# Optimization experiments

Measured on AMD Instinct MI355X. Metric: run time of the kernel, lower is better.

The kernel has to match this reference:

```python
import jax, jax.numpy as jnp
import numpy as np

N_NODES = 50000
N_EDGES = 1600000
DIM = 512


def setup_inputs() -> dict:
    key = jax.random.key(0)
    k1, k2, k3, k4, k5 = jax.random.split(key, 5)
    x = jax.random.normal(k1, (N_NODES, DIM), dtype=jnp.float32)
    adj_rows = jax.random.randint(k2, (N_EDGES,), 0, N_NODES, dtype=jnp.int32)
    adj_cols = jax.random.randint(k3, (N_EDGES,), 0, N_NODES, dtype=jnp.int32)
    adj_vals = jax.random.uniform(k4, (N_EDGES,), dtype=jnp.float32)
    # fc1 weight [out_dim, in_dim], kaiming-normal-ish init
    weight = jax.random.normal(k5, (DIM, DIM), dtype=jnp.float32) * np.float32(np.sqrt(2.0 / DIM))
    scale = jnp.full((1,), 1.5, dtype=jnp.float32)
    return {"x": x, "adj_rows": adj_rows, "adj_cols": adj_cols,
            "adj_vals": adj_vals, "weight": weight, "scale": scale}


def reference(x, adj_rows, adj_cols, adj_vals, weight, scale):
    # dropout in eval mode -> identity
    N, D = x.shape
    # dense linear: y = x @ W^T
    y = jnp.einsum('nd,od->no', x, weight)
    # sparse adj @ y  (COO SpMM via gather + segment_sum)
    y = jax.ops.segment_sum(adj_vals[:, None] * y[adj_cols], adj_rows,
                            num_segments=N)
    # sp_norm: mean-center over nodes, scale by global RMS^{-1} * (1+scale) * sqrt(D)
    y_t = y - jnp.mean(y, axis=0, keepdims=True)
    y_norm = jnp.mean(jnp.sum(y_t * y_t, axis=1)) ** -0.5
    y = y_t * y_norm * (1.0 + scale) * jnp.float32(np.sqrt(D))
    # activation (relu), then residual (input_dim == output_dim)
    y = jax.nn.relu(y)
    return y + x
```

## Files before the change

### kernel.cpp

```cpp
#include <hip/hip_runtime.h>
#include <hip/hip_bf16.h>
#include <cstdint>
#include <cstddef>

#define N_NODES 50000
#define DIM 512
#define N_EDGES 1600000
#define NT 25
#define NB (N_NODES * NT)
#define GPANELS 391
#define NSHAD 8

typedef __bf16 bf16;
typedef __bf16 bf16x8 __attribute__((ext_vector_type(8)));
typedef __bf16 bf16x4 __attribute__((ext_vector_type(4)));
typedef float floatx4 __attribute__((ext_vector_type(4)));

__global__ void cast_kernel(const float* __restrict__ in, bf16* __restrict__ out, int n4) {
    int i = blockIdx.x * blockDim.x + threadIdx.x;
    if (i >= n4) return;
    float4 v = reinterpret_cast<const float4*>(in)[i];
    bf16x4 o;
    o[0] = (bf16)v.x; o[1] = (bf16)v.y; o[2] = (bf16)v.z; o[3] = (bf16)v.w;
    reinterpret_cast<bf16x4*>(out)[i] = o;
}

__global__ void hist_kernel(const int* __restrict__ rows, const int* __restrict__ cols,
                            int* __restrict__ cnt, int E) {
    int i = blockIdx.x * blockDim.x + threadIdx.x;
    if (i < E) {
        int key = rows[i] * NT + (cols[i] >> 11);
        atomicAdd(&cnt[key], 1);
    }
}

__global__ __launch_bounds__(1024) void scanA_kernel(const int* __restrict__ cnt,
                                                     int* __restrict__ row_start,
                                                     int* __restrict__ blksum, int n) {
    const int t = threadIdx.x;
    int i = blockIdx.x * 1024 + t;
    int v = (i < n) ? cnt[i] : 0;
    int s = v;
#pragma unroll
    for (int off = 1; off < 64; off <<= 1) {
        int u = __shfl_up(s, off, 64);
        if ((t & 63) >= off) s += u;
    }
    __shared__ int wsum[16];
    if ((t & 63) == 63) wsum[t >> 6] = s;
    __syncthreads();
    if (t < 16) {
        int w = wsum[t];
#pragma unroll
        for (int off = 1; off < 16; off <<= 1) {
            int u = __shfl_up(w, off, 16);
            if (t >= off) w += u;
        }
        wsum[t] = w;
    }
    __syncthreads();
    int base = (t >= 64) ? wsum[(t >> 6) - 1] : 0;
    int incl = s + base;
    if (i < n) row_start[i] = incl - v;
    if (t == 1023) blksum[blockIdx.x] = incl;
}

__global__ __launch_bounds__(1024) void scanB_kernel(const int* __restrict__ blksum,
                                                     int* __restrict__ blkoff, int nb) {
    __shared__ int s[1024];
    const int t = threadIdx.x;
    const int base = t * 2;
    int a = (base < nb) ? blksum[base] : 0;
    int b = (base + 1 < nb) ? blksum[base + 1] : 0;
    s[t] = a + b;
    __syncthreads();
    for (int off = 1; off < 1024; off <<= 1) {
        int u = (t >= off) ? s[t - off] : 0;
        __syncthreads();
        s[t] += u;
        __syncthreads();
    }
    int excl = (t == 0) ? 0 : s[t - 1];
    if (base < nb) blkoff[base] = excl;
    if (base + 1 < nb) blkoff[base + 1] = excl + a;
}

__global__ __launch_bounds__(1024) void scanC_kernel(int* __restrict__ row_start,
                                                     const int* __restrict__ blkoff,
                                                     int* __restrict__ cursor, int n) {
    int i = blockIdx.x * 1024 + threadIdx.x;
    if (i >= n) return;
    int v = row_start[i] + blkoff[i >> 10];
    row_start[i] = v;
    cursor[i] = v;
    if (i == n - 1) row_start[n] = N_EDGES;
}

__global__ void scatter_kernel(const int* __restrict__ rows, const int* __restrict__ cols,
                               const float* __restrict__ vals, int* __restrict__ cursor,
                               int2* __restrict__ ecv, int E) {
    int i = blockIdx.x * blockDim.x + threadIdx.x;
    if (i >= E) return;
    int c = cols[i];
    int key = rows[i] * NT + (c >> 11);
    int p = atomicAdd(&cursor[key], 1);
    ecv[p] = make_int2(c, __float_as_int(vals[i]));
}

__global__ __launch_bounds__(256) void gemm_kernel(const bf16* __restrict__ A,
                                                   const bf16* __restrict__ B,
                                                   bf16* __restrict__ C) {
    __shared__ bf16 lA[128 * 32];
    __shared__ bf16 lB[128 * 32];
    const int d = blockIdx.x;
    const int p = (d & 7) + ((d >> 5) << 3);
    const int c = (d >> 3) & 3;
    if (p >= GPANELS) return;
    const int t = threadIdx.x;
    const int wave = t >> 6;
    const int lane = t & 63;
    const int rowBase = p * 128;
    const int colBase = c * 128;
    const int wm = (wave >> 1) * 64;
    const int wn = (wave & 1) * 64;
    floatx4 acc[4][4] = {};

    const int r_a = t >> 2;
    const int kk = (t & 3) * 8;

    const int l15 = lane & 15;
    const int koff = (lane >> 4) * 8;

    for (int k0 = 0; k0 < DIM; k0 += 32) {
#pragma unroll
        for (int j = 0; j < 2; j++) {
            int row = rowBase + r_a + j * 64;
            if (row > N_NODES - 1) row = N_NODES - 1;
            const bf16* g = A + (size_t)row * DIM + k0 + kk;
            bf16* l = lA + wave * 512 + j * 2048;
            __builtin_amdgcn_global_load_lds(
                (const __attribute__((address_space(1))) void*)g,
                (__attribute__((address_space(3))) void*)l, 16, 0, 0);
        }
#pragma unroll
        for (int j = 0; j < 2; j++) {
            int row = colBase + r_a + j * 64;
            const bf16* g = B + (size_t)row * DIM + k0 + kk;
            bf16* l = lB + wave * 512 + j * 2048;
            __builtin_amdgcn_global_load_lds(
                (const __attribute__((address_space(1))) void*)g,
                (__attribute__((address_space(3))) void*)l, 16, 0, 0);
        }
        __syncthreads();
        bf16x8 af[4], bfr[4];
#pragma unroll
        for (int i = 0; i < 4; i++)
            af[i] = *reinterpret_cast<const bf16x8*>(lA + (wm + i * 16 + l15) * 32 + koff);
#pragma unroll
        for (int j = 0; j < 4; j++)
            bfr[j] = *reinterpret_cast<const bf16x8*>(lB + (wn + j * 16 + l15) * 32 + koff);
#pragma unroll
        for (int i = 0; i < 4; i++)
#pragma unroll
            for (int j = 0; j < 4; j++)
                acc[i][j] = __builtin_amdgcn_mfma_f32_16x16x32_bf16(af[i], bfr[j], acc[i][j], 0, 0, 0);
        __syncthreads();
    }
    const int rquad = (lane >> 4) * 4;
#pragma unroll
    for (int i = 0; i < 4; i++) {
#pragma unroll
        for (int reg = 0; reg < 4; reg++) {
            int gr = rowBase + wm + i * 16 + rquad + reg;
            if (gr >= N_NODES) continue;
#pragma unroll
            for (int j = 0; j < 4; j++) {
                int gc = colBase + wn + j * 16 + l15;
                C[(size_t)gr * DIM + gc] = (bf16)acc[i][j][reg];
            }
        }
    }
}

__device__ __forceinline__ float blo(uint32_t w) { return __uint_as_float(w << 16); }
__device__ __forceinline__ float bhi(uint32_t w) { return __uint_as_float(w & 0xffff0000u); }

__device__ __forceinline__ void fmac8(float* acc, float v, const uint4& w) {
    acc[0] += v * blo(w.x); acc[1] += v * bhi(w.x);
    acc[2] += v * blo(w.y); acc[3] += v * bhi(w.y);
    acc[4] += v * blo(w.z); acc[5] += v * bhi(w.z);
    acc[6] += v * blo(w.w); acc[7] += v * bhi(w.w);
}

__global__ __launch_bounds__(256) void spmm_kernel(const int* __restrict__ row_start,
                                                   const int2* __restrict__ ecv,
                                                   const bf16* __restrict__ y,
                                                   float* __restrict__ y2) {
    const int wave = threadIdx.x >> 6;
    const int lane = threadIdx.x & 63;
    const int r = blockIdx.x * 4 + wave;
    const int s = row_start[r * NT];
    const int e = row_start[(r + 1) * NT];
    float acc[8] = {0.f, 0.f, 0.f, 0.f, 0.f, 0.f, 0.f, 0.f};
    const uint32_t* yb = reinterpret_cast<const uint32_t*>(y);

    int i = s;
    for (; i + 3 < e; i += 4) {
        int2 e0 = ecv[i], e1 = ecv[i + 1], e2 = ecv[i + 2], e3 = ecv[i + 3];
        uint4 w0 = *reinterpret_cast<const uint4*>(yb + (size_t)e0.x * 256 + lane * 4);
        uint4 w1 = *reinterpret_cast<const uint4*>(yb + (size_t)e1.x * 256 + lane * 4);
        uint4 w2 = *reinterpret_cast<const uint4*>(yb + (size_t)e2.x * 256 + lane * 4);
        uint4 w3 = *reinterpret_cast<const uint4*>(yb + (size_t)e3.x * 256 + lane * 4);
        fmac8(acc, __int_as_float(e0.y), w0);
        fmac8(acc, __int_as_float(e1.y), w1);
        fmac8(acc, __int_as_float(e2.y), w2);
        fmac8(acc, __int_as_float(e3.y), w3);
    }
    for (; i < e; i++) {
        int2 e0 = ecv[i];
        uint4 w0 = *reinterpret_cast<const uint4*>(yb + (size_t)e0.x * 256 + lane * 4);
        fmac8(acc, __int_as_float(e0.y), w0);
    }
    float4* out = reinterpret_cast<float4*>(y2 + (size_t)r * DIM + lane * 8);
    out[0] = make_float4(acc[0], acc[1], acc[2], acc[3]);
    out[1] = make_float4(acc[4], acc[5], acc[6], acc[7]);
}

#define RED_GRID 512
#define RED_CHUNK 16
__global__ __launch_bounds__(256) void reduce_kernel(const float* __restrict__ y2,
                                                     float* __restrict__ colsumS,
                                                     float* __restrict__ totsqS) {
    const int t = threadIdx.x;
    const int d2 = t * 2;
    float c0 = 0.f, c1 = 0.f, sq = 0.f;
    for (int r0 = blockIdx.x * RED_CHUNK; r0 < N_NODES; r0 += RED_GRID * RED_CHUNK) {
        float2 v[RED_CHUNK];
#pragma unroll
        for (int j = 0; j < RED_CHUNK; j++) {
            int r = r0 + j;
            v[j] = (r < N_NODES)
                       ? *reinterpret_cast<const float2*>(y2 + (size_t)r * DIM + d2)
                       : make_float2(0.f, 0.f);
        }
#pragma unroll
        for (int j = 0; j < RED_CHUNK; j++) {
            c0 += v[j].x;
            c1 += v[j].y;
            sq += v[j].x * v[j].x + v[j].y * v[j].y;
        }
    }
    const int sh = blockIdx.x & (NSHAD - 1);
    atomicAdd(&colsumS[sh * DIM + d2], c0);
    atomicAdd(&colsumS[sh * DIM + d2 + 1], c1);
    __shared__ float ssq[256];
    ssq[t] = sq;
    __syncthreads();
    for (int off = 128; off > 0; off >>= 1) {
        if (t < off) ssq[t] += ssq[t + off];
        __syncthreads();
    }
    if (t == 0) atomicAdd(&totsqS[sh], ssq[0]);
}

__global__ void scalar_kernel(const float* __restrict__ colsumS, const float* __restrict__ totsqS,
                              const float* __restrict__ scale, float* __restrict__ sfac,
                              float* __restrict__ colsum) {
    __shared__ float sm[512];
    const int t = threadIdx.x;
    float s = 0.f;
#pragma unroll
    for (int c = 0; c < NSHAD; c++) s += colsumS[c * DIM + t];
    colsum[t] = s;
    float mu = s * (1.0f / N_NODES);
    sm[t] = mu * mu;
    __syncthreads();
    for (int off = 256; off > 0; off >>= 1) {
        if (t < off) sm[t] += sm[t + off];
        __syncthreads();
    }
    if (t == 0) {
        float tq = 0.f;
#pragma unroll
        for (int c = 0; c < NSHAD; c++) tq += totsqS[c];
        float var = tq * (1.0f / N_NODES) - sm[0];
        sfac[0] = rsqrtf(var) * (1.0f + scale[0]) * sqrtf((float)DIM);
    }
}

__global__ void final_kernel(float* __restrict__ y2, const float* __restrict__ x,
                             const float* __restrict__ colsum, const float* __restrict__ sfac,
                             int n4) {
    int i = blockIdx.x * blockDim.x + threadIdx.x;
    if (i >= n4) return;
    const float invN = 1.0f / N_NODES;
    float4 v = reinterpret_cast<float4*>(y2)[i];
    float4 xv = reinterpret_cast<const float4*>(x)[i];
    float4 mu = reinterpret_cast<const float4*>(colsum)[i & 127];
    float s = sfac[0];
    v.x = fmaxf((v.x - mu.x * invN) * s, 0.0f) + xv.x;
    v.y = fmaxf((v.y - mu.y * invN) * s, 0.0f) + xv.y;
    v.z = fmaxf((v.z - mu.z * invN) * s, 0.0f) + xv.z;
    v.w = fmaxf((v.w - mu.w * invN) * s, 0.0f) + xv.w;
    reinterpret_cast<float4*>(y2)[i] = v;
}

extern "C" void kernel_launch(void* const* d_in, const int* in_sizes, int n_in,
                              void* d_out, int out_size, void* d_ws, size_t ws_size,
                              hipStream_t stream) {
    const float* x        = (const float*)d_in[0];
    const int*   adj_rows = (const int*)d_in[1];
    const int*   adj_cols = (const int*)d_in[2];
    const float* adj_vals = (const float*)d_in[3];
    const float* weight   = (const float*)d_in[4];
    const float* scale    = (const float*)d_in[5];
    float* out = (float*)d_out;

    char* ws = (char*)d_ws;
    size_t off = 0;
    auto alloc = [&](size_t b) {
        char* p = ws + off;
        off += (b + 255) & ~(size_t)255;
        return p;
    };
    const int nblk = (NB + 1023) / 1024;
    bf16*  xb        = (bf16*)alloc((size_t)N_NODES * DIM * 2);
    int2*  ecv       = (int2*)xb;
    bf16*  Wb        = (bf16*)alloc((size_t)DIM * DIM * 2);
    bf16*  y         = (bf16*)alloc((size_t)N_NODES * DIM * 2);
    int*   cnt       = (int*)alloc((size_t)NB * 4);
    int*   cursor    = cnt;
    int*   row_start = (int*)alloc((size_t)(NB + 1) * 4);
    int*   blksum    = (int*)alloc((size_t)nblk * 4);
    int*   blkoff    = (int*)alloc((size_t)nblk * 4);
    float* colsumS   = (float*)alloc((size_t)NSHAD * DIM * 4);
    float* totsqS    = (float*)alloc((size_t)NSHAD * 4);
    float* colsum    = (float*)alloc(512 * 4);
    float* sfac      = (float*)alloc(4);
    (void)ws_size; (void)in_sizes; (void)n_in; (void)out_size;

    hipMemsetAsync(cnt, 0, (size_t)NB * 4, stream);
    hipMemsetAsync(colsumS, 0, (size_t)NSHAD * DIM * 4 + 256, stream);

    const int n4x = N_NODES * DIM / 4;
    const int n4w = DIM * DIM / 4;
    cast_kernel<<<(n4x + 255) / 256, 256, 0, stream>>>(x, xb, n4x);
    cast_kernel<<<(n4w + 255) / 256, 256, 0, stream>>>(weight, Wb, n4w);

    gemm_kernel<<<1568, 256, 0, stream>>>(xb, Wb, y);

    hist_kernel<<<(N_EDGES + 255) / 256, 256, 0, stream>>>(adj_rows, adj_cols, cnt, N_EDGES);
    scanA_kernel<<<nblk, 1024, 0, stream>>>(cnt, row_start, blksum, NB);
    scanB_kernel<<<1, 1024, 0, stream>>>(blksum, blkoff, nblk);
    scanC_kernel<<<nblk, 1024, 0, stream>>>(row_start, blkoff, cursor, NB);
    scatter_kernel<<<(N_EDGES + 255) / 256, 256, 0, stream>>>(adj_rows, adj_cols, adj_vals,
                                                              cursor, ecv, N_EDGES);

    spmm_kernel<<<N_NODES / 4, 256, 0, stream>>>(row_start, ecv, y, out);

    reduce_kernel<<<RED_GRID, 256, 0, stream>>>(out, colsumS, totsqS);
    scalar_kernel<<<1, 512, 0, stream>>>(colsumS, totsqS, scale, sfac, colsum);
    final_kernel<<<(n4x + 255) / 256, 256, 0, stream>>>(out, x, colsum, sfac, n4x);
}
```

Baseline: 684.9 us.

## Double-buffer GEMM LDS tiles and fuse casts and memsets into one prep kernel

The bf16 GEMM now keeps two LDS buffers. It issues the global-to-LDS loads for the next K slice before computing MFMAs on the current one, and the K loop is fully unrolled. The goal is to hide global load latency behind the matrix math, at the cost of doubling LDS use per block, which may lower occupancy. Separately, the two cast launches and the two hipMemsetAsync calls are merged into a single prep kernel that casts x and W and zeroes the histogram and statistics buffers, removing launch and memset overhead.

```diff
diff --git a/kernel.cpp b/kernel.cpp
--- a/kernel.cpp
+++ b/kernel.cpp
@@ -16,13 +16,25 @@
 typedef __bf16 bf16x4 __attribute__((ext_vector_type(4)));
 typedef float floatx4 __attribute__((ext_vector_type(4)));
 
-__global__ void cast_kernel(const float* __restrict__ in, bf16* __restrict__ out, int n4) {
+__global__ void prep_kernel(const float* __restrict__ x, bf16* __restrict__ xb,
+                            const float* __restrict__ w, bf16* __restrict__ wb,
+                            int4* __restrict__ cnt4, float4* __restrict__ stats4,
+                            int n4x, int n4w) {
     int i = blockIdx.x * blockDim.x + threadIdx.x;
-    if (i >= n4) return;
-    float4 v = reinterpret_cast<const float4*>(in)[i];
-    bf16x4 o;
-    o[0] = (bf16)v.x; o[1] = (bf16)v.y; o[2] = (bf16)v.z; o[3] = (bf16)v.w;
-    reinterpret_cast<bf16x4*>(out)[i] = o;
+    if (i < n4x) {
+        float4 v = reinterpret_cast<const float4*>(x)[i];
+        bf16x4 o;
+        o[0] = (bf16)v.x; o[1] = (bf16)v.y; o[2] = (bf16)v.z; o[3] = (bf16)v.w;
+        reinterpret_cast<bf16x4*>(xb)[i] = o;
+    }
+    if (i < n4w) {
+        float4 v = reinterpret_cast<const float4*>(w)[i];
+        bf16x4 o;
+        o[0] = (bf16)v.x; o[1] = (bf16)v.y; o[2] = (bf16)v.z; o[3] = (bf16)v.w;
+        reinterpret_cast<bf16x4*>(wb)[i] = o;
+    }
+    if (i < NB / 4) cnt4[i] = make_int4(0, 0, 0, 0);
+    if (i < 1026) stats4[i] = make_float4(0.f, 0.f, 0.f, 0.f);
 }
 
 __global__ void hist_kernel(const int* __restrict__ rows, const int* __restrict__ cols,
@@ -110,8 +122,8 @@
 __global__ __launch_bounds__(256) void gemm_kernel(const bf16* __restrict__ A,
                                                    const bf16* __restrict__ B,
                                                    bf16* __restrict__ C) {
-    __shared__ bf16 lA[128 * 32];
-    __shared__ bf16 lB[128 * 32];
+    __shared__ bf16 lA[2][128 * 32];
+    __shared__ bf16 lB[2][128 * 32];
     const int d = blockIdx.x;
     const int p = (d & 7) + ((d >> 5) << 3);
     const int c = (d >> 3) & 3;
@@ -127,38 +139,47 @@
 
     const int r_a = t >> 2;
     const int kk = (t & 3) * 8;
-
     const int l15 = lane & 15;
     const int koff = (lane >> 4) * 8;
 
-    for (int k0 = 0; k0 < DIM; k0 += 32) {
-#pragma unroll
-        for (int j = 0; j < 2; j++) {
-            int row = rowBase + r_a + j * 64;
-            if (row > N_NODES - 1) row = N_NODES - 1;
-            const bf16* g = A + (size_t)row * DIM + k0 + kk;
-            bf16* l = lA + wave * 512 + j * 2048;
-            __builtin_amdgcn_global_load_lds(
-                (const __attribute__((address_space(1))) void*)g,
-                (__attribute__((address_space(3))) void*)l, 16, 0, 0);
-        }
-#pragma unroll
-        for (int j = 0; j < 2; j++) {
-            int row = colBase + r_a + j * 64;
-            const bf16* g = B + (size_t)row * DIM + k0 + kk;
-            bf16* l = lB + wave * 512 + j * 2048;
-            __builtin_amdgcn_global_load_lds(
-                (const __attribute__((address_space(1))) void*)g,
-                (__attribute__((address_space(3))) void*)l, 16, 0, 0);
-        }
-        __syncthreads();
+    int arow0 = rowBase + r_a;
+    if (arow0 > N_NODES - 1) arow0 = N_NODES - 1;
+    int arow1 = rowBase + r_a + 64;
+    if (arow1 > N_NODES - 1) arow1 = N_NODES - 1;
+    const bf16* gA0 = A + (size_t)arow0 * DIM + kk;
+    const bf16* gA1 = A + (size_t)arow1 * DIM + kk;
+    const bf16* gB0 = B + (size_t)(colBase + r_a) * DIM + kk;
+    const bf16* gB1 = B + (size_t)(colBase + r_a + 64) * DIM + kk;
+
+    auto STAGE = [&](int b, int kc) {
+        const int ko = kc * 32;
+        __builtin_amdgcn_global_load_lds(
+            (const __attribute__((address_space(1))) void*)(gA0 + ko),
+            (__attribute__((address_space(3))) void*)(&lA[b][wave * 512]), 16, 0, 0);
+        __builtin_amdgcn_global_load_lds(
+            (const __attribute__((address_space(1))) void*)(gA1 + ko),
+            (__attribute__((address_space(3))) void*)(&lA[b][wave * 512 + 2048]), 16, 0, 0);
+        __builtin_amdgcn_global_load_lds(
+            (const __attribute__((address_space(1))) void*)(gB0 + ko),
+            (__attribute__((address_space(3))) void*)(&lB[b][wave * 512]), 16, 0, 0);
+        __builtin_amdgcn_global_load_lds(
+            (const __attribute__((address_space(1))) void*)(gB1 + ko),
+            (__attribute__((address_space(3))) void*)(&lB[b][wave * 512 + 2048]), 16, 0, 0);
+    };
+
+    STAGE(0, 0);
+    __syncthreads();
+#pragma unroll
+    for (int s = 0; s < 16; s++) {
+        if (s + 1 < 16) STAGE((s + 1) & 1, s + 1);
+        const int b = s & 1;
         bf16x8 af[4], bfr[4];
 #pragma unroll
         for (int i = 0; i < 4; i++)
-            af[i] = *reinterpret_cast<const bf16x8*>(lA + (wm + i * 16 + l15) * 32 + koff);
+            af[i] = *reinterpret_cast<const bf16x8*>(&lA[b][(wm + i * 16 + l15) * 32 + koff]);
 #pragma unroll
         for (int j = 0; j < 4; j++)
-            bfr[j] = *reinterpret_cast<const bf16x8*>(lB + (wn + j * 16 + l15) * 32 + koff);
+            bfr[j] = *reinterpret_cast<const bf16x8*>(&lB[b][(wn + j * 16 + l15) * 32 + koff]);
 #pragma unroll
         for (int i = 0; i < 4; i++)
 #pragma unroll
@@ -339,13 +360,12 @@
     float* sfac      = (float*)alloc(4);
     (void)ws_size; (void)in_sizes; (void)n_in; (void)out_size;
 
-    hipMemsetAsync(cnt, 0, (size_t)NB * 4, stream);
-    hipMemsetAsync(colsumS, 0, (size_t)NSHAD * DIM * 4 + 256, stream);
-
     const int n4x = N_NODES * DIM / 4;
     const int n4w = DIM * DIM / 4;
-    cast_kernel<<<(n4x + 255) / 256, 256, 0, stream>>>(x, xb, n4x);
-    cast_kernel<<<(n4w + 255) / 256, 256, 0, stream>>>(weight, Wb, n4w);
+
+    prep_kernel<<<(n4x + 255) / 256, 256, 0, stream>>>(x, xb, weight, Wb,
+                                                       (int4*)cnt, (float4*)colsumS,
+                                                       n4x, n4w);
 
     gemm_kernel<<<1568, 256, 0, stream>>>(xb, Wb, y);
 
```

New measurement: 700.1 us. +2.2%, slower.
